# Optimization experiments

Hardware: AMD Instinct MI355X
Metric: run time of the kernel (lower is better)

Reference implementation:

```python
import jax, jax.numpy as jnp
import numpy as np

N, E, D, G, L, C, NI, NL = 100000, 1600000, 128, 1024, 3, 128, 100000, 64


def setup_inputs() -> dict:
    key = jax.random.key(0)
    ks = jax.random.split(key, 16)
    x = jax.random.normal(ks[0], (N, D), dtype=jnp.float32)
    src = jax.random.randint(ks[1], (E,), 0, N, dtype=jnp.int32)
    dst = jax.random.randint(ks[2], (E,), 0, N, dtype=jnp.int32)
    graph_ids = jnp.sort(jax.random.randint(ks[3], (N,), 0, G, dtype=jnp.int32))
    init_feat = jax.random.normal(ks[4], (NI, D), dtype=jnp.float32)
    init_graph_ids = jnp.sort(jax.random.randint(ks[5], (NI,), 0, G, dtype=jnp.int32))
    lead_feat = jax.random.normal(ks[6], (NL, D), dtype=jnp.float32)
    s = 1.0 / np.sqrt(D)
    W = jax.random.normal(ks[7], (L, D, D), dtype=jnp.float32) * s
    Wc = jax.random.normal(ks[8], (L, D, D), dtype=jnp.float32) * s
    b = jnp.zeros((L, D), dtype=jnp.float32)
    eps = jnp.zeros((L,), dtype=jnp.float32)
    fc1_w = jax.random.normal(ks[9], (D, D), dtype=jnp.float32) * s
    fc1_b = jnp.zeros((D,), dtype=jnp.float32)
    fc2_w = jax.random.normal(ks[10], (D, C), dtype=jnp.float32) * s
    fc2_b = jnp.zeros((C,), dtype=jnp.float32)
    return {"x": x, "src": src, "dst": dst, "graph_ids": graph_ids,
            "init_feat": init_feat, "init_graph_ids": init_graph_ids,
            "lead_feat": lead_feat, "W": W, "Wc": Wc, "b": b, "eps": eps,
            "fc1_w": fc1_w, "fc1_b": fc1_b, "fc2_w": fc2_w, "fc2_b": fc2_b,
            "num_graphs": G}


def reference(x, src, dst, graph_ids, init_feat, init_graph_ids, lead_feat,
              W, Wc, b, eps, fc1_w, fc1_b, fc2_w, fc2_b, num_graphs):
    n_nodes = x.shape[0]
    # global context: per-graph sum pooling of initial graph + lead graph sum
    h_init = jax.ops.segment_sum(init_feat, init_graph_ids, num_segments=num_graphs)  # [G,D]
    h_lead = jnp.sum(lead_feat, axis=0)  # [D]
    ctx = h_init[graph_ids] + h_lead  # [N,D], constant across layers

    h = x
    h_global = jax.ops.segment_sum(h, graph_ids, num_segments=num_graphs)  # [G,D]
    for l in range(W.shape[0]):
        agg = jax.ops.segment_sum(h[src], dst, num_segments=n_nodes)  # neighbor sum [N,D]
        m = (1.0 + eps[l]) * h + agg + h_global[graph_ids]
        h = jax.nn.relu(m @ W[l] + ctx @ Wc[l] + b[l])
        h_global = jax.ops.segment_sum(h, graph_ids, num_segments=num_graphs)
    out = jax.nn.relu(h_global @ fc1_w + fc1_b) @ fc2_w + fc2_b  # [G,C]
    return out
```

## Files before the change

### kernel.cpp

```cpp
#include <hip/hip_runtime.h>

#define D 128

typedef short short8_t __attribute__((ext_vector_type(8)));
typedef float float4_t __attribute__((ext_vector_type(4)));

#define BSH 8
#define BSZ 256
#define NBLK_A 256

__device__ __forceinline__ float bf_lo(unsigned u) { return __uint_as_float(u << 16); }
__device__ __forceinline__ float bf_hi(unsigned u) { return __uint_as_float(u & 0xffff0000u); }
__device__ __forceinline__ unsigned to_bf1(float x) {
    unsigned b = __float_as_uint(x);
    return (b + 0x7fffu + ((b >> 16) & 1u)) >> 16;
}
__device__ __forceinline__ unsigned pack2(float a, float b) {
    return to_bf1(a) | (to_bf1(b) << 16);
}

__global__ __launch_bounds__(256)
void prep1(const int* __restrict__ dst, int* __restrict__ Hist, int E_, int chunk,
           const float4* __restrict__ x4, uint2* __restrict__ xb2, long n4,
           const float* __restrict__ W, uint4* __restrict__ Wpk, int L_,
           const int* __restrict__ gids, int N_, const int* __restrict__ init_gid, int NI_,
           int G_, int* __restrict__ nstart, int* __restrict__ istart,
           const float* __restrict__ leadf, int NL_, float* __restrict__ hlead,
           int eb1, int eb2, int eb3) {
    int b = blockIdx.x, t = threadIdx.x;
    if (b < NBLK_A) {
        __shared__ int h[512];
        h[t] = 0; h[t + 256] = 0;
        __syncthreads();
        int base = b * chunk;
        int end = base + chunk; if (end > E_) end = E_;
        for (int i = base + t; i < end; i += 256)
            atomicAdd(&h[dst[i] >> BSH], 1);
        __syncthreads();
        Hist[b * 512 + t] = h[t];
        Hist[b * 512 + t + 256] = h[t + 256];
    } else if (b < eb1) {
        long i = (long)(b - NBLK_A) * 256 + t;
        long stride = (long)(eb1 - NBLK_A) * 256;
        for (; i < n4; i += stride) {
            float4 v = x4[i];
            xb2[i] = make_uint2(pack2(v.x, v.y), pack2(v.z, v.w));
        }
    } else if (b < eb2) {
        int id = (b - eb1) * 256 + t;
        if (id < L_ * 2048) {
            int lane = id & 63, cc = (id >> 6) & 3, tt = (id >> 8) & 7, l = id >> 11;
            int n = tt * 16 + (lane & 15);
            int k0 = cc * 32 + (lane >> 4) * 8;
            const float* Wb = W + (long)l * D * D;
            unsigned u0 = pack2(Wb[(long)(k0 + 0) * D + n], Wb[(long)(k0 + 1) * D + n]);
            unsigned u1 = pack2(Wb[(long)(k0 + 2) * D + n], Wb[(long)(k0 + 3) * D + n]);
            unsigned u2 = pack2(Wb[(long)(k0 + 4) * D + n], Wb[(long)(k0 + 5) * D + n]);
            unsigned u3 = pack2(Wb[(long)(k0 + 6) * D + n], Wb[(long)(k0 + 7) * D + n]);
            Wpk[id] = make_uint4(u0, u1, u2, u3);
        }
    } else if (b < eb3) {
        int id = (b - eb2) * 256 + t;
        if (id < 2 * (G_ + 1)) {
            const int* arr; int n; int* outp; int g;
            if (id <= G_) { arr = gids; n = N_; outp = nstart; g = id; }
            else { arr = init_gid; n = NI_; outp = istart; g = id - (G_ + 1); }
            if (g == G_) outp[g] = n;
            else {
                int lo = 0, hi = n;
                while (lo < hi) { int mid = (lo + hi) >> 1; if (arr[mid] < g) lo = mid + 1; else hi = mid; }
                outp[g] = lo;
            }
        }
    } else {
        if (t < D) {
            float a0 = 0.f, a1 = 0.f, a2 = 0.f, a3 = 0.f;
            int r = 0;
            for (; r + 4 <= NL_; r += 4) {
                a0 += leadf[(long)r * D + t];
                a1 += leadf[(long)(r + 1) * D + t];
                a2 += leadf[(long)(r + 2) * D + t];
                a3 += leadf[(long)(r + 3) * D + t];
            }
            for (; r < NL_; ++r) a0 += leadf[(long)r * D + t];
            hlead[t] = a0 + a1 + a2 + a3;
        }
    }
}


__global__ __launch_bounds__(256)
void csr_scan_blocks(int* __restrict__ Hist, int* __restrict__ Tot) {
    __shared__ int sc[256];
    int bkt = blockIdx.x, t = threadIdx.x;
    int v = Hist[t * 512 + bkt];
    sc[t] = v; __syncthreads();
    for (int off = 1; off < 256; off <<= 1) {
        int u = (t >= off) ? sc[t - off] : 0;
        __syncthreads();
        sc[t] += u;
        __syncthreads();
    }
    Hist[t * 512 + bkt] = sc[t] - v;
    if (t == 255) Tot[bkt] = sc[255];
}

__global__ __launch_bounds__(512)
void csr_scan_base(const int* __restrict__ Tot, int* __restrict__ Base, int NB) {
    __shared__ int sc[512];
    int t = threadIdx.x;
    int v = (t < NB) ? Tot[t] : 0;
    sc[t] = v; __syncthreads();
    for (int off = 1; off < 512; off <<= 1) {
        int u = (t >= off) ? sc[t - off] : 0;
        __syncthreads();
        sc[t] += u;
        __syncthreads();
    }
    Base[t] = sc[t] - v;
    if (t == NB - 1) Base[NB] = sc[t];
}

__global__ __launch_bounds__(256)
void phase3(const int* __restrict__ src, const int* __restrict__ dst,
            const int* __restrict__ Hist, const int* __restrict__ Base,
            unsigned* __restrict__ EdgeBuf, int E_, int chunk,
            const float* __restrict__ initf, const int* __restrict__ istart,
            const float* __restrict__ hlead, float* __restrict__ cvec, int G_) {
    int b = blockIdx.x, t = threadIdx.x;
    if (b < NBLK_A) {
        __shared__ int cur[512];
        cur[t]       = Base[t]       + Hist[b * 512 + t];
        cur[t + 256] = Base[t + 256] + Hist[b * 512 + t + 256];
        __syncthreads();
        int base = b * chunk;
        int end = base + chunk; if (end > E_) end = E_;
        for (int i = base + t; i < end; i += 256) {
            int s = src[i], dd = dst[i];
            int p = atomicAdd(&cur[dd >> BSH], 1);
            EdgeBuf[p] = (unsigned)s | ((unsigned)(dd & (BSZ - 1)) << 24);
        }
        return;
    }
    int g = b - NBLK_A;
    if (g >= G_) return;
    __shared__ float xs2[2][D];
    int col = t & 127, rp = t >> 7;
    int r0 = istart[g], r1 = istart[g + 1];
    float a0 = 0.f, a1 = 0.f, a2 = 0.f, a3 = 0.f;
    int r = r0 + rp;
    for (; r + 6 < r1; r += 8) {
        a0 += initf[(long)r * D + col];
        a1 += initf[(long)(r + 2) * D + col];
        a2 += initf[(long)(r + 4) * D + col];
        a3 += initf[(long)(r + 6) * D + col];
    }
    for (; r < r1; r += 2) a0 += initf[(long)r * D + col];
    xs2[rp][col] = (a0 + a1) + (a2 + a3);
    __syncthreads();
    if (t < D) cvec[(long)g * D + t] = xs2[0][t] + xs2[1][t] + hlead[t];
}

__global__ __launch_bounds__(256)
void csr_fill(const unsigned* __restrict__ EdgeBuf, const int* __restrict__ Base,
              int* __restrict__ rowptr, int* __restrict__ csr, int N_, int E_) {
    __shared__ int deg[256];
    __shared__ int cur[256];
    int b = blockIdx.x, t = threadIdx.x;
    int e0 = Base[b], e1 = Base[b + 1];
    deg[t] = 0;
    __syncthreads();
    for (int i = e0 + t; i < e1; i += 256)
        atomicAdd(&deg[EdgeBuf[i] >> 24], 1);
    __syncthreads();
    int v = deg[t];
    cur[t] = v; __syncthreads();
    for (int off = 1; off < 256; off <<= 1) {
        int u = (t >= off) ? cur[t - off] : 0;
        __syncthreads();
        cur[t] += u;
        __syncthreads();
    }
    int excl = cur[t] - v;
    int node = b * BSZ + t;
    if (node < N_) rowptr[node] = e0 + excl;
    cur[t] = e0 + excl;
    __syncthreads();
    for (int i = e0 + t; i < e1; i += 256) {
        unsigned ev = EdgeBuf[i];
        int p = atomicAdd(&cur[ev >> 24], 1);
        csr[p] = (int)(ev & 0x00FFFFFFu);
    }
    if (b == 0 && t == 0) rowptr[N_] = E_;
}

__global__ __launch_bounds__(128)
void graph_side(const unsigned* __restrict__ hb, const int* __restrict__ start,
                const float* __restrict__ cvec, const float* __restrict__ Wl,
                const float* __restrict__ Wcl, const float* __restrict__ bl,
                float* __restrict__ T) {
    __shared__ float xs[D];
    __shared__ float cs[D];
    int g = blockIdx.x, tid = threadIdx.x;
    int r0 = start[g], r1 = start[g + 1];
    int c = tid >> 1;
    bool hi = tid & 1;
    float a0=0,a1=0,a2=0,a3=0,a4=0,a5=0,a6=0,a7=0;
    int r = r0;
    for (; r + 8 <= r1; r += 8) {
        unsigned u0 = hb[(long)(r+0)*64+c], u1 = hb[(long)(r+1)*64+c];
        unsigned u2 = hb[(long)(r+2)*64+c], u3 = hb[(long)(r+3)*64+c];
        unsigned u4 = hb[(long)(r+4)*64+c], u5 = hb[(long)(r+5)*64+c];
        unsigned u6 = hb[(long)(r+6)*64+c], u7 = hb[(long)(r+7)*64+c];
        a0 += hi ? bf_hi(u0) : bf_lo(u0);
        a1 += hi ? bf_hi(u1) : bf_lo(u1);
        a2 += hi ? bf_hi(u2) : bf_lo(u2);
        a3 += hi ? bf_hi(u3) : bf_lo(u3);
        a4 += hi ? bf_hi(u4) : bf_lo(u4);
        a5 += hi ? bf_hi(u5) : bf_lo(u5);
        a6 += hi ? bf_hi(u6) : bf_lo(u6);
        a7 += hi ? bf_hi(u7) : bf_lo(u7);
    }
    for (; r < r1; ++r) {
        unsigned u = hb[(long)r*64+c];
        a0 += hi ? bf_hi(u) : bf_lo(u);
    }
    xs[tid] = ((a0+a1)+(a2+a3)) + ((a4+a5)+(a6+a7));
    cs[tid] = cvec[(long)g * D + tid];
    __syncthreads();
    float p0=0,p1=0,p2=0,p3=0;
    for (int k = 0; k < D; k += 4) {
        p0 += xs[k]   * Wl[(long)k*D + tid];
        p1 += xs[k+1] * Wl[(long)(k+1)*D + tid];
        p2 += xs[k+2] * Wl[(long)(k+2)*D + tid];
        p3 += xs[k+3] * Wl[(long)(k+3)*D + tid];
    }
    for (int k = 0; k < D; k += 4) {
        p0 += cs[k]   * Wcl[(long)k*D + tid];
        p1 += cs[k+1] * Wcl[(long)(k+1)*D + tid];
        p2 += cs[k+2] * Wcl[(long)(k+2)*D + tid];
        p3 += cs[k+3] * Wcl[(long)(k+3)*D + tid];
    }
    T[(long)g * D + tid] = bl[tid] + (p0 + p1) + (p2 + p3);
}

__global__ __launch_bounds__(128)
void readout(const unsigned* __restrict__ hb, const int* __restrict__ start,
             const float* __restrict__ f1w, const float* __restrict__ f1b,
             const float* __restrict__ f2w, const float* __restrict__ f2b,
             float* __restrict__ out) {
    __shared__ float part[2][64][2];
    __shared__ float xs[D];
    __shared__ float zs[D];
    int g = blockIdx.x, t = threadIdx.x;
    int c = t & 63, half = t >> 6;
    int r0 = start[g], r1 = start[g + 1];
    float l0=0,h0=0,l1=0,h1=0;
    int r = r0 + half;
    for (; r + 2 < r1; r += 4) {
        unsigned a = hb[(long)r * 64 + c];
        unsigned bq = hb[(long)(r + 2) * 64 + c];
        l0 += bf_lo(a);  h0 += bf_hi(a);
        l1 += bf_lo(bq); h1 += bf_hi(bq);
    }
    if (r < r1) { unsigned a = hb[(long)r * 64 + c]; l0 += bf_lo(a); h0 += bf_hi(a); }
    part[half][c][0] = l0 + l1;
    part[half][c][1] = h0 + h1;
    __syncthreads();
    xs[t] = part[0][t >> 1][t & 1] + part[1][t >> 1][t & 1];
    __syncthreads();
    float p0=0,p1=0,p2=0,p3=0;
    for (int k = 0; k < D; k += 4) {
        p0 += xs[k]     * f1w[(long)k * D + t];
        p1 += xs[k + 1] * f1w[(long)(k + 1) * D + t];
        p2 += xs[k + 2] * f1w[(long)(k + 2) * D + t];
        p3 += xs[k + 3] * f1w[(long)(k + 3) * D + t];
    }
    zs[t] = fmaxf(f1b[t] + (p0 + p1) + (p2 + p3), 0.f);
    __syncthreads();
    float q0=0,q1=0,q2=0,q3=0;
    for (int k = 0; k < D; k += 4) {
        q0 += zs[k]     * f2w[(long)k * D + t];
        q1 += zs[k + 1] * f2w[(long)(k + 1) * D + t];
        q2 += zs[k + 2] * f2w[(long)(k + 2) * D + t];
        q3 += zs[k + 3] * f2w[(long)(k + 3) * D + t];
    }
    out[(long)g * D + t] = f2b[t] + (q0 + q1) + (q2 + q3);
}

#define TROWS 64
__global__ __launch_bounds__(256, 6)
void layer_kernel(const unsigned* __restrict__ hb, const uint4* __restrict__ Wpk_l,
                  const float* __restrict__ T, const int* __restrict__ gids,
                  const int* __restrict__ rowptr, const int* __restrict__ csr,
                  const float* __restrict__ eps_l, unsigned* __restrict__ houtb, int n) {
    __shared__ __align__(16) unsigned Minb[TROWS][68];
    int tid = threadIdx.x;
    int w = tid >> 6, lane = tid & 63;
    int w16 = w * 16;
    int rowBase = blockIdx.x * TROWS;
    int rb = rowBase + w16;
    float epsv = 1.0f + *eps_l;

    int rp = rb + lane; if (rp > n) rp = n;
    int evv = rowptr[rp];

    int e0 = __shfl(evv, 0);
    int e1 = __shfl(evv, 1);
    int idxv = (e0 + lane < e1) ? csr[e0 + lane] : 0;

    for (int i = 0; i < 16; ++i) {
        int r = rb + i;
        int deg = e1 - e0;
        int e0n = __shfl(evv, i + 1);
        int e1n = __shfl(evv, i + 2);
        int idxn = (e0n + lane < e1n) ? csr[e0n + lane] : 0;
        float sx = 0.f, sy = 0.f;
        if (r < n) {
            unsigned su = hb[(long)r * 64 + lane];
            float ax0 = epsv * bf_lo(su), ay0 = epsv * bf_hi(su);
            float ax1=0,ay1=0,ax2=0,ay2=0,ax3=0,ay3=0;
            int iv = idxv;
            int base = 0;
            while (true) {
                int m = deg - base; if (m > 64) m = 64;
                int j = 0;
                for (; j + 8 <= m; j += 8) {
                    int s0=__shfl(iv,j+0), s1=__shfl(iv,j+1), s2=__shfl(iv,j+2), s3=__shfl(iv,j+3);
                    int s4=__shfl(iv,j+4), s5=__shfl(iv,j+5), s6=__shfl(iv,j+6), s7=__shfl(iv,j+7);
                    unsigned u0=hb[(long)s0*64+lane], u1=hb[(long)s1*64+lane];
                    unsigned u2=hb[(long)s2*64+lane], u3=hb[(long)s3*64+lane];
                    unsigned u4=hb[(long)s4*64+lane], u5=hb[(long)s5*64+lane];
                    unsigned u6=hb[(long)s6*64+lane], u7=hb[(long)s7*64+lane];
                    ax0+=bf_lo(u0); ay0+=bf_hi(u0); ax1+=bf_lo(u1); ay1+=bf_hi(u1);
                    ax2+=bf_lo(u2); ay2+=bf_hi(u2); ax3+=bf_lo(u3); ay3+=bf_hi(u3);
                    ax0+=bf_lo(u4); ay0+=bf_hi(u4); ax1+=bf_lo(u5); ay1+=bf_hi(u5);
                    ax2+=bf_lo(u6); ay2+=bf_hi(u6); ax3+=bf_lo(u7); ay3+=bf_hi(u7);
                }
                for (; j < m; ++j) {
                    int s = __shfl(iv, j);
                    unsigned u = hb[(long)s * 64 + lane];
                    ax0 += bf_lo(u); ay0 += bf_hi(u);
                }
                base += 64;
                if (base >= deg) break;
                int mm = deg - base;
                iv = (lane < mm) ? csr[e0 + base + lane] : 0;
            }
            sx = (ax0 + ax1) + (ax2 + ax3);
            sy = (ay0 + ay1) + (ay2 + ay3);
        }
        Minb[w16 + i][lane] = pack2(sx, sy);
        e0 = e0n; e1 = e1n; idxv = idxn;
    }

    int m_ = lane & 15, quad = lane >> 4;
    float4_t acc[8];
    #pragma unroll
    for (int tt = 0; tt < 8; ++tt) { acc[tt][0]=0.f; acc[tt][1]=0.f; acc[tt][2]=0.f; acc[tt][3]=0.f; }

    #pragma unroll
    for (int cc = 0; cc < 4; ++cc) {
        short8_t af = *(const short8_t*)&Minb[w16 + m_][cc * 16 + quad * 4];
        #pragma unroll
        for (int tt = 0; tt < 8; ++tt) {
            short8_t bf = *(const short8_t*)&Wpk_l[(tt * 4 + cc) * 64 + lane];
            acc[tt] = __builtin_amdgcn_mfma_f32_16x16x32_bf16(af, bf, acc[tt], 0, 0, 0);
        }
    }

    int gq[4];
    #pragma unroll
    for (int reg = 0; reg < 4; ++reg) {
        int r = rb + quad * 4 + reg;
        gq[reg] = (r < n) ? gids[r] : 0;
    }
    #pragma unroll
    for (int tt = 0; tt < 8; ++tt) {
        int col = tt * 16 + m_;
        #pragma unroll
        for (int reg = 0; reg < 4; ++reg) {
            float v = acc[tt][reg] + T[(long)gq[reg] * D + col];
            v = fmaxf(v, 0.f);
            float v2 = __shfl_xor(v, 1);
            if (!(lane & 1)) Minb[w16 + quad * 4 + reg][tt * 8 + (m_ >> 1)] = pack2(v, v2);
        }
    }
    #pragma unroll
    for (int rr = 0; rr < 4; ++rr) {
        int lrow = rr * 4 + (lane >> 4);
        int r = rowBase + w16 + lrow;
        if (r < n) {
            uint4 v = *(const uint4*)&Minb[w16 + lrow][(lane & 15) * 4];
            *(uint4*)&houtb[(long)r * 64 + (lane & 15) * 4] = v;
        }
    }
}


static inline size_t align512(size_t x) { return (x + 511) & ~(size_t)511; }

extern "C" void kernel_launch(void* const* d_in, const int* in_sizes, int n_in,
                              void* d_out, int out_size, void* d_ws, size_t ws_size,
                              hipStream_t stream) {
    const float* x        = (const float*)d_in[0];
    const int*   src      = (const int*)d_in[1];
    const int*   dst      = (const int*)d_in[2];
    const int*   gids     = (const int*)d_in[3];
    const float* initf    = (const float*)d_in[4];
    const int*   init_gid = (const int*)d_in[5];
    const float* leadf    = (const float*)d_in[6];
    const float* W        = (const float*)d_in[7];
    const float* Wc       = (const float*)d_in[8];
    const float* b        = (const float*)d_in[9];
    const float* eps      = (const float*)d_in[10];
    const float* fc1_w    = (const float*)d_in[11];
    const float* fc1_b    = (const float*)d_in[12];
    const float* fc2_w    = (const float*)d_in[13];
    const float* fc2_b    = (const float*)d_in[14];
    float* out = (float*)d_out;

    const int N  = in_sizes[0] / D;
    const int E  = in_sizes[1];
    const int NI = in_sizes[4] / D;
    const int NL = in_sizes[6] / D;
    const int L  = in_sizes[10];
    const int C  = in_sizes[13] / D;
    const int G  = out_size / C;

    char* p = (char*)d_ws;
    unsigned* xb  = (unsigned*)p; p += align512((size_t)N * 64 * 4);
    unsigned* hAb = (unsigned*)p; p += align512((size_t)N * 64 * 4);
    unsigned* hBb = (unsigned*)p; p += align512((size_t)N * 64 * 4);
    float* T     = (float*)p; p += align512((size_t)G * D * 4);
    float* cvec  = (float*)p; p += align512((size_t)G * D * 4);
    float* hlead = (float*)p; p += align512((size_t)D * 4);
    int* rowptr  = (int*)p;   p += align512((size_t)(N + 1) * 4);
    int* csr     = (int*)p;   p += align512((size_t)E * 4);
    unsigned* EdgeBuf = (unsigned*)p; p += align512((size_t)E * 4);
    int* Hist    = (int*)p;   p += align512((size_t)NBLK_A * 512 * 4);
    int* Tot     = (int*)p;   p += align512((size_t)520 * 4);
    int* Base    = (int*)p;   p += align512((size_t)520 * 4);
    int* nstart  = (int*)p;   p += align512((size_t)(G + 1) * 4);
    int* istart  = (int*)p;   p += align512((size_t)(G + 1) * 4);
    uint4* Wpk   = (uint4*)p; p += align512((size_t)L * 2048 * 16);
    (void)ws_size; (void)n_in;

    const int NB = (N + BSZ - 1) / BSZ;
    const int chunk = (E + NBLK_A - 1) / NBLK_A;

    const int CVB = 2048;
    const int WPB = (L * 2048 + 255) / 256;
    const int STB = (2 * (G + 1) + 255) / 256;
    const int eb1 = NBLK_A + CVB;
    const int eb2 = eb1 + WPB;
    const int eb3 = eb2 + STB;
    const int prepBlocks = eb3 + 1;

    prep1<<<prepBlocks, 256, 0, stream>>>(dst, Hist, E, chunk,
                                          (const float4*)x, (uint2*)xb, (long)N * D / 4,
                                          W, Wpk, L,
                                          gids, N, init_gid, NI, G, nstart, istart,
                                          leadf, NL, hlead, eb1, eb2, eb3);
    csr_scan_blocks<<<NB, 256, 0, stream>>>(Hist, Tot);
    csr_scan_base<<<1, 512, 0, stream>>>(Tot, Base, NB);
    phase3<<<NBLK_A + G, 256, 0, stream>>>(src, dst, Hist, Base, EdgeBuf, E, chunk,
                                           initf, istart, hlead, cvec, G);
    csr_fill<<<NB, 256, 0, stream>>>(EdgeBuf, Base, rowptr, csr, N, E);

    const unsigned* hcur = xb;
    unsigned* bufs[2] = { hAb, hBb };
    int layerBlocks = (N + TROWS - 1) / TROWS;
    for (int l = 0; l < L; ++l) {
        graph_side<<<G, D, 0, stream>>>(hcur, nstart, cvec, W + (long)l * D * D,
                                        Wc + (long)l * D * D, b + (long)l * D, T);
        unsigned* hnext = bufs[l & 1];
        layer_kernel<<<layerBlocks, 256, 0, stream>>>(hcur, Wpk + (size_t)l * 2048, T,
                                                      gids, rowptr, csr,
                                                      eps + l, hnext, N);
        hcur = hnext;
    }

    readout<<<G, D, 0, stream>>>(hcur, nstart, fc1_w, fc1_b, fc2_w, fc2_b, out);
}
```

Baseline: 491.1 us.

## Fuse per-graph sum pooling into layer kernel epilogue via atomics

Per-graph feature sums are now accumulated in fp32 inside the layer kernel's epilogue using wavefront shuffles and atomicAdd into a G×D buffer, instead of being recomputed by graph_side and readout re-reading the whole bf16 h array. The initial pooling of x is added as extra blocks in phase3, and T_gemm zeroes the next accumulator. This removes three full passes over N×D node features, at the cost of atomic traffic and a per-graph loop in the layer epilogue. It also changes numerics: sums are taken from fp32 pre-rounding values and the initial pool uses fp32 x rather than bf16.

Measured after the change: 594.8 us. 21.1% more time.

```diff
diff --git a/kernel.cpp b/kernel.cpp
--- a/kernel.cpp
+++ b/kernel.cpp
@@ -126,7 +126,9 @@
             const int* __restrict__ Hist, const int* __restrict__ Base,
             unsigned* __restrict__ EdgeBuf, int E_, int chunk,
             const float* __restrict__ initf, const int* __restrict__ istart,
-            const float* __restrict__ hlead, float* __restrict__ cvec, int G_) {
+            const float* __restrict__ hlead, float* __restrict__ cvec,
+            const float* __restrict__ x, const int* __restrict__ nstart,
+            float* __restrict__ hg0, int G_) {
     int b = blockIdx.x, t = threadIdx.x;
     if (b < NBLK_A) {
         __shared__ int cur[512];
@@ -143,22 +145,28 @@
         return;
     }
     int g = b - NBLK_A;
-    if (g >= G_) return;
+    const float* feat; const int* st; const float* addv; float* outp;
+    if (g < G_) { feat = initf; st = istart; addv = hlead; outp = cvec; }
+    else { g -= G_; if (g >= G_) return; feat = x; st = nstart; addv = nullptr; outp = hg0; }
     __shared__ float xs2[2][D];
     int col = t & 127, rp = t >> 7;
-    int r0 = istart[g], r1 = istart[g + 1];
+    int r0 = st[g], r1 = st[g + 1];
     float a0 = 0.f, a1 = 0.f, a2 = 0.f, a3 = 0.f;
     int r = r0 + rp;
     for (; r + 6 < r1; r += 8) {
-        a0 += initf[(long)r * D + col];
-        a1 += initf[(long)(r + 2) * D + col];
-        a2 += initf[(long)(r + 4) * D + col];
-        a3 += initf[(long)(r + 6) * D + col];
-    }
-    for (; r < r1; r += 2) a0 += initf[(long)r * D + col];
+        a0 += feat[(long)r * D + col];
+        a1 += feat[(long)(r + 2) * D + col];
+        a2 += feat[(long)(r + 4) * D + col];
+        a3 += feat[(long)(r + 6) * D + col];
+    }
+    for (; r < r1; r += 2) a0 += feat[(long)r * D + col];
     xs2[rp][col] = (a0 + a1) + (a2 + a3);
     __syncthreads();
-    if (t < D) cvec[(long)g * D + t] = xs2[0][t] + xs2[1][t] + hlead[t];
+    if (t < D) {
+        float s = xs2[0][t] + xs2[1][t];
+        if (addv) s += addv[t];
+        outp[(long)g * D + t] = s;
+    }
 }
 
 __global__ __launch_bounds__(256)
@@ -195,38 +203,16 @@
 }
 
 __global__ __launch_bounds__(128)
-void graph_side(const unsigned* __restrict__ hb, const int* __restrict__ start,
-                const float* __restrict__ cvec, const float* __restrict__ Wl,
-                const float* __restrict__ Wcl, const float* __restrict__ bl,
-                float* __restrict__ T) {
+void T_gemm(const float* __restrict__ hg, const float* __restrict__ cvec,
+            const float* __restrict__ Wl, const float* __restrict__ Wcl,
+            const float* __restrict__ bl, float* __restrict__ T,
+            float* __restrict__ hgz) {
     __shared__ float xs[D];
     __shared__ float cs[D];
     int g = blockIdx.x, tid = threadIdx.x;
-    int r0 = start[g], r1 = start[g + 1];
-    int c = tid >> 1;
-    bool hi = tid & 1;
-    float a0=0,a1=0,a2=0,a3=0,a4=0,a5=0,a6=0,a7=0;
-    int r = r0;
-    for (; r + 8 <= r1; r += 8) {
-        unsigned u0 = hb[(long)(r+0)*64+c], u1 = hb[(long)(r+1)*64+c];
-        unsigned u2 = hb[(long)(r+2)*64+c], u3 = hb[(long)(r+3)*64+c];
-        unsigned u4 = hb[(long)(r+4)*64+c], u5 = hb[(long)(r+5)*64+c];
-        unsigned u6 = hb[(long)(r+6)*64+c], u7 = hb[(long)(r+7)*64+c];
-        a0 += hi ? bf_hi(u0) : bf_lo(u0);
-        a1 += hi ? bf_hi(u1) : bf_lo(u1);
-        a2 += hi ? bf_hi(u2) : bf_lo(u2);
-        a3 += hi ? bf_hi(u3) : bf_lo(u3);
-        a4 += hi ? bf_hi(u4) : bf_lo(u4);
-        a5 += hi ? bf_hi(u5) : bf_lo(u5);
-        a6 += hi ? bf_hi(u6) : bf_lo(u6);
-        a7 += hi ? bf_hi(u7) : bf_lo(u7);
-    }
-    for (; r < r1; ++r) {
-        unsigned u = hb[(long)r*64+c];
-        a0 += hi ? bf_hi(u) : bf_lo(u);
-    }
-    xs[tid] = ((a0+a1)+(a2+a3)) + ((a4+a5)+(a6+a7));
+    xs[tid] = hg[(long)g * D + tid];
     cs[tid] = cvec[(long)g * D + tid];
+    hgz[(long)g * D + tid] = 0.f;
     __syncthreads();
     float p0=0,p1=0,p2=0,p3=0;
     for (int k = 0; k < D; k += 4) {
@@ -245,29 +231,14 @@
 }
 
 __global__ __launch_bounds__(128)
-void readout(const unsigned* __restrict__ hb, const int* __restrict__ start,
+void readout(const float* __restrict__ hg,
              const float* __restrict__ f1w, const float* __restrict__ f1b,
              const float* __restrict__ f2w, const float* __restrict__ f2b,
              float* __restrict__ out) {
-    __shared__ float part[2][64][2];
     __shared__ float xs[D];
     __shared__ float zs[D];
     int g = blockIdx.x, t = threadIdx.x;
-    int c = t & 63, half = t >> 6;
-    int r0 = start[g], r1 = start[g + 1];
-    float l0=0,h0=0,l1=0,h1=0;
-    int r = r0 + half;
-    for (; r + 2 < r1; r += 4) {
-        unsigned a = hb[(long)r * 64 + c];
-        unsigned bq = hb[(long)(r + 2) * 64 + c];
-        l0 += bf_lo(a);  h0 += bf_hi(a);
-        l1 += bf_lo(bq); h1 += bf_hi(bq);
-    }
-    if (r < r1) { unsigned a = hb[(long)r * 64 + c]; l0 += bf_lo(a); h0 += bf_hi(a); }
-    part[half][c][0] = l0 + l1;
-    part[half][c][1] = h0 + h1;
-    __syncthreads();
-    xs[t] = part[0][t >> 1][t & 1] + part[1][t >> 1][t & 1];
+    xs[t] = hg[(long)g * D + t];
     __syncthreads();
     float p0=0,p1=0,p2=0,p3=0;
     for (int k = 0; k < D; k += 4) {
@@ -293,7 +264,8 @@
 void layer_kernel(const unsigned* __restrict__ hb, const uint4* __restrict__ Wpk_l,
                   const float* __restrict__ T, const int* __restrict__ gids,
                   const int* __restrict__ rowptr, const int* __restrict__ csr,
-                  const float* __restrict__ eps_l, unsigned* __restrict__ houtb, int n) {
+                  const float* __restrict__ eps_l, unsigned* __restrict__ houtb,
+                  float* __restrict__ hgNext, int n) {
     __shared__ __align__(16) unsigned Minb[TROWS][68];
     int tid = threadIdx.x;
     int w = tid >> 6, lane = tid & 63;
@@ -369,11 +341,13 @@
         }
     }
 
-    int gq[4];
+    int gq[4]; int gm[4];
     #pragma unroll
     for (int reg = 0; reg < 4; ++reg) {
         int r = rb + quad * 4 + reg;
-        gq[reg] = (r < n) ? gids[r] : 0;
+        bool ok = r < n;
+        gq[reg] = ok ? gids[r] : 0;
+        gm[reg] = ok ? gq[reg] : -1;
     }
     #pragma unroll
     for (int tt = 0; tt < 8; ++tt) {
@@ -382,6 +356,7 @@
         for (int reg = 0; reg < 4; ++reg) {
             float v = acc[tt][reg] + T[(long)gq[reg] * D + col];
             v = fmaxf(v, 0.f);
+            acc[tt][reg] = v;
             float v2 = __shfl_xor(v, 1);
             if (!(lane & 1)) Minb[w16 + quad * 4 + reg][tt * 8 + (m_ >> 1)] = pack2(v, v2);
         }
@@ -393,6 +368,28 @@
         if (r < n) {
             uint4 v = *(const uint4*)&Minb[w16 + lrow][(lane & 15) * 4];
             *(uint4*)&houtb[(long)r * 64 + (lane & 15) * 4] = v;
+        }
+    }
+
+    if (rb < n) {
+        int gfirst = gids[rb];
+        int rlast = rb + 15 < n ? rb + 15 : n - 1;
+        int glast = gids[rlast];
+        for (int g = gfirst; g <= glast; ++g) {
+            float ps[8];
+            #pragma unroll
+            for (int tt = 0; tt < 8; ++tt) {
+                float s = 0.f;
+                #pragma unroll
+                for (int reg = 0; reg < 4; ++reg)
+                    s += (gm[reg] == g) ? acc[tt][reg] : 0.f;
+                s += __shfl_xor(s, 16);
+                s += __shfl_xor(s, 32);
+                ps[tt] = s;
+            }
+            int t0 = 2 * quad, t1 = 2 * quad + 1;
+            atomicAdd(&hgNext[(long)g * D + t0 * 16 + m_], ps[t0]);
+            atomicAdd(&hgNext[(long)g * D + t1 * 16 + m_], ps[t1]);
         }
     }
 }
@@ -434,6 +431,8 @@
     unsigned* hBb = (unsigned*)p; p += align512((size_t)N * 64 * 4);
     float* T     = (float*)p; p += align512((size_t)G * D * 4);
     float* cvec  = (float*)p; p += align512((size_t)G * D * 4);
+    float* hgA   = (float*)p; p += align512((size_t)G * D * 4);
+    float* hgB   = (float*)p; p += align512((size_t)G * D * 4);
     float* hlead = (float*)p; p += align512((size_t)D * 4);
     int* rowptr  = (int*)p;   p += align512((size_t)(N + 1) * 4);
     int* csr     = (int*)p;   p += align512((size_t)E * 4);
@@ -464,22 +463,26 @@
                                           leadf, NL, hlead, eb1, eb2, eb3);
     csr_scan_blocks<<<NB, 256, 0, stream>>>(Hist, Tot);
     csr_scan_base<<<1, 512, 0, stream>>>(Tot, Base, NB);
-    phase3<<<NBLK_A + G, 256, 0, stream>>>(src, dst, Hist, Base, EdgeBuf, E, chunk,
-                                           initf, istart, hlead, cvec, G);
+    phase3<<<NBLK_A + 2 * G, 256, 0, stream>>>(src, dst, Hist, Base, EdgeBuf, E, chunk,
+                                               initf, istart, hlead, cvec,
+                                               x, nstart, hgA, G);
     csr_fill<<<NB, 256, 0, stream>>>(EdgeBuf, Base, rowptr, csr, N, E);
 
     const unsigned* hcur = xb;
     unsigned* bufs[2] = { hAb, hBb };
+    float* hgCur = hgA;
+    float* hgNext = hgB;
     int layerBlocks = (N + TROWS - 1) / TROWS;
     for (int l = 0; l < L; ++l) {
-        graph_side<<<G, D, 0, stream>>>(hcur, nstart, cvec, W + (long)l * D * D,
-                                        Wc + (long)l * D * D, b + (long)l * D, T);
+        T_gemm<<<G, D, 0, stream>>>(hgCur, cvec, W + (long)l * D * D,
+                                    Wc + (long)l * D * D, b + (long)l * D, T, hgNext);
         unsigned* hnext = bufs[l & 1];
         layer_kernel<<<layerBlocks, 256, 0, stream>>>(hcur, Wpk + (size_t)l * 2048, T,
                                                       gids, rowptr, csr,
-                                                      eps + l, hnext, N);
+                                                      eps + l, hnext, hgNext, N);
         hcur = hnext;
-    }
-
-    readout<<<G, D, 0, stream>>>(hcur, nstart, fc1_w, fc1_b, fc2_w, fc2_b, out);
-}
+        float* tmp = hgCur; hgCur = hgNext; hgNext = tmp;
+    }
+
+    readout<<<G, D, 0, stream>>>(hgCur, fc1_w, fc1_b, fc2_w, fc2_b, out);
+}
```
